# Optimization experiments

Measured on AMD Instinct MI355X. Metric: run time of the kernel, lower is better.

Reference implementation:

```python
import jax, jax.numpy as jnp
import numpy as np

S, B, H2, V = 2048, 16, 2048, 1024  # seq, batch, 2*hidden_dim, v_dim
ALPHA_S = 0.5


def setup_inputs() -> dict:
    key = jax.random.key(0)
    ks = jax.random.split(key, 8)
    sc_in = 1.0 / np.sqrt(H2)
    sc_v = 1.0 / np.sqrt(V)
    return {
        "hidden": jax.random.normal(ks[0], (S, B, H2), dtype=jnp.float32),
        "z": jax.random.normal(ks[1], (S, B, H2), dtype=jnp.float32),
        "Ww": jax.random.normal(ks[2], (H2, V), dtype=jnp.float32) * sc_in,
        "bw": jax.random.normal(ks[3], (V,), dtype=jnp.float32) * sc_in,
        "Wz": jax.random.normal(ks[4], (H2, V), dtype=jnp.float32) * sc_in,
        "bz": jax.random.normal(ks[5], (V,), dtype=jnp.float32) * sc_in,
        "Vw": jax.random.normal(ks[6], (V, 1), dtype=jnp.float32) * sc_v,
        "vb": jax.random.normal(ks[7], (1,), dtype=jnp.float32) * sc_v,
        "w_a": jnp.zeros((), dtype=jnp.float32),
    }


def reference(hidden, z, Ww, bw, Wz, bz, Vw, vb, w_a):
    # sum_w = w_w(hidden) + w_z(z) + w_a * alpha_s   -> [S, B, V]
    sum_w = (jnp.einsum("sbh,hv->sbv", hidden, Ww) + bw
             + jnp.einsum("sbh,hv->sbv", z, Wz) + bz
             + w_a * ALPHA_S)
    # u = v(tanh(sum_w))                              -> [S, B, 1]
    u = jnp.einsum("sbv,vo->sbo", jnp.tanh(sum_w), Vw) + vb
    # softmax over the sequence (dim 0)
    attention = jax.nn.softmax(u, axis=0)
    return attention
```

## Files before the change

kernel.cpp:

```cpp
#include <hip/hip_runtime.h>
#include <hip/hip_bf16.h>
#include <stdint.h>

#define S_DIM 2048
#define B_DIM 16
#define H2_DIM 2048
#define V_DIM 1024
#define M_DIM (S_DIM * B_DIM)
#define K_HALF 2048
#define K_TOT 4096

typedef __attribute__((ext_vector_type(8))) short s16x8;
typedef __attribute__((ext_vector_type(4))) float f32x4;

__device__ __forceinline__ uint16_t f2bf(float f) {
    union { float f; uint32_t u; } c; c.f = f;
    uint32_t u = c.u;
    u += 0x7fffu + ((u >> 16) & 1u);
    return (uint16_t)(u >> 16);
}

__device__ __forceinline__ uint32_t pack_bf16_rn(float a, float b) {
    union { float f; uint32_t u; } ca, cb; ca.f = a; cb.f = b;
    uint32_t ua = ca.u + 0x8000u;
    uint32_t ub = cb.u + 0x8000u;
    return __builtin_amdgcn_perm(ub, ua, 0x07060302u);
}

__device__ __forceinline__ float fast_tanh(float x) {
    float e = __expf(2.0f * x);
    return 1.0f - 2.0f / (e + 1.0f);
}

__device__ __forceinline__ void gload_lds16(const void* g, void* l) {
    __builtin_amdgcn_global_load_lds(
        (__attribute__((address_space(1))) void*)(uintptr_t)g,
        (__attribute__((address_space(3))) void*)(uint32_t)(uintptr_t)l,
        16, 0, 0);
}

__global__ void transposeB(const float* __restrict__ Ww, const float* __restrict__ Wz,
                           uint16_t* __restrict__ B1, uint16_t* __restrict__ B2) {
    __shared__ float tile[32][33];
    const float* src = blockIdx.z ? Wz : Ww;
    uint16_t* dst = blockIdx.z ? B2 : B1;
    int k0 = blockIdx.x * 32, v0 = blockIdx.y * 32;
    int tv = threadIdx.x & 31, tk = threadIdx.x >> 5;
#pragma unroll
    for (int r = 0; r < 4; r++) {
        int k = tk * 4 + r;
        tile[k][tv] = src[(size_t)(k0 + k) * V_DIM + v0 + tv];
    }
    __syncthreads();
#pragma unroll
    for (int r = 0; r < 4; r++) {
        int v = tk * 4 + r;
        dst[(size_t)(v0 + v) * K_HALF + k0 + tv] = f2bf(tile[tv][v]);
    }
}

__global__ __launch_bounds__(256, 2) void gemm_kernel(
    const float* __restrict__ F1, const float* __restrict__ F2,
    const uint16_t* __restrict__ B1, const uint16_t* __restrict__ B2,
    const float* __restrict__ bw, const float* __restrict__ bz,
    const float* __restrict__ wa_p, const float* __restrict__ Vw,
    float* __restrict__ u) {
    __shared__ __align__(16) uint16_t lA[128 * 64];
    __shared__ __align__(16) uint16_t lB[256 * 64];

    const int tid = threadIdx.x;
    const int lane = tid & 63;
    const int wv = tid >> 6;
    const int wm = (wv >> 1) * 64, wn = (wv & 1) * 128;
    const int id = blockIdx.x;
    const int nBase = ((id >> 3) & 3) * 256;
    const int mBase = ((id & 7) + ((id >> 5) << 3)) * 128;
    const int lr = lane >> 3;
    const int lc = lane & 7;
    const int cg = lc ^ lr;
    const int col = lane & 15, quad = lane >> 4;

    f32x4 acc[4][8] = {};

    for (int kb = 0; kb < K_TOT; kb += 64) {
        const int kcol = kb & (K_HALF - 1);
        const float* Fb = (kb < K_HALF) ? F1 : F2;
        const uint16_t* Bb = (kb < K_HALF) ? B1 : B2;

        __syncthreads();

#pragma unroll
        for (int j = 0; j < 8; j++) {
            const int rb = wv * 64 + j * 8;
            const uint16_t* gb = Bb + (size_t)(nBase + rb + lr) * K_HALF + kcol + cg * 8;
            gload_lds16(gb, &lB[rb * 64]);
        }
#pragma unroll
        for (int j = 0; j < 4; j++) {
            const int rb = wv * 32 + j * 8;
            const float* gp = Fb + (size_t)(mBase + rb + lr) * K_HALF + kcol + cg * 8;
            float4 x = ((const float4*)gp)[0];
            float4 y = ((const float4*)gp)[1];
            uint32_t p0 = pack_bf16_rn(x.x, x.y);
            uint32_t p1 = pack_bf16_rn(x.z, x.w);
            uint32_t p2 = pack_bf16_rn(y.x, y.y);
            uint32_t p3 = pack_bf16_rn(y.z, y.w);
            *(uint4*)&lA[rb * 64 + lane * 8] = make_uint4(p0, p1, p2, p3);
        }
        __syncthreads();

#pragma unroll
        for (int kk = 0; kk < 2; kk++) {
            s16x8 af[4], bf[8];
            const int cidx = kk * 4 + quad;
#pragma unroll
            for (int i = 0; i < 4; i++) {
                int m = wm + i * 16 + col;
                af[i] = *(const s16x8*)&lA[m * 64 + ((cidx ^ (m & 7)) << 3)];
            }
#pragma unroll
            for (int j = 0; j < 8; j++) {
                int n = wn + j * 16 + col;
                bf[j] = *(const s16x8*)&lB[n * 64 + ((cidx ^ (n & 7)) << 3)];
            }
#pragma unroll
            for (int i = 0; i < 4; i++)
#pragma unroll
                for (int j = 0; j < 8; j++)
                    acc[i][j] = __builtin_amdgcn_mfma_f32_16x16x32_bf16(af[i], bf[j], acc[i][j], 0, 0, 0);
        }
    }

    const float wa05 = wa_p[0] * 0.5f;
    float biasv[8], vwv[8];
#pragma unroll
    for (int j = 0; j < 8; j++) {
        int n = nBase + wn + j * 16 + col;
        biasv[j] = bw[n] + bz[n] + wa05;
        vwv[j] = Vw[n];
    }
#pragma unroll
    for (int i = 0; i < 4; i++) {
#pragma unroll
        for (int r = 0; r < 4; r++) {
            float s = 0.f;
#pragma unroll
            for (int j = 0; j < 8; j++) {
                float xv = acc[i][j][r] + biasv[j];
                s += fast_tanh(xv) * vwv[j];
            }
            s += __shfl_xor(s, 8);
            s += __shfl_xor(s, 4);
            s += __shfl_xor(s, 2);
            s += __shfl_xor(s, 1);
            if (col == 0)
                atomicAdd(&u[mBase + wm + i * 16 + quad * 4 + r], s);
        }
    }
}

__global__ void softmax_kernel(float* __restrict__ u) {
    const int b = blockIdx.x;
    const int t = threadIdx.x;
    __shared__ float redm[4], reds[4];
    float v[8];
    float mx = -1e30f;
#pragma unroll
    for (int k = 0; k < 8; k++) {
        v[k] = u[(size_t)(t + k * 256) * B_DIM + b];
        mx = fmaxf(mx, v[k]);
    }
#pragma unroll
    for (int off = 32; off >= 1; off >>= 1) mx = fmaxf(mx, __shfl_xor(mx, off));
    if ((t & 63) == 0) redm[t >> 6] = mx;
    __syncthreads();
    mx = fmaxf(fmaxf(redm[0], redm[1]), fmaxf(redm[2], redm[3]));
    float s = 0.f;
#pragma unroll
    for (int k = 0; k < 8; k++) {
        v[k] = __expf(v[k] - mx);
        s += v[k];
    }
#pragma unroll
    for (int off = 32; off >= 1; off >>= 1) s += __shfl_xor(s, off);
    if ((t & 63) == 0) reds[t >> 6] = s;
    __syncthreads();
    s = reds[0] + reds[1] + reds[2] + reds[3];
    float inv = 1.0f / s;
#pragma unroll
    for (int k = 0; k < 8; k++)
        u[(size_t)(t + k * 256) * B_DIM + b] = v[k] * inv;
}

extern "C" void kernel_launch(void* const* d_in, const int* in_sizes, int n_in,
                              void* d_out, int out_size, void* d_ws, size_t ws_size,
                              hipStream_t stream) {
    const float* hidden = (const float*)d_in[0];
    const float* z = (const float*)d_in[1];
    const float* Ww = (const float*)d_in[2];
    const float* bw = (const float*)d_in[3];
    const float* Wz = (const float*)d_in[4];
    const float* bz = (const float*)d_in[5];
    const float* Vw = (const float*)d_in[6];
    const float* wa = (const float*)d_in[8];
    float* out = (float*)d_out;

    char* ws = (char*)d_ws;
    const size_t bBytes = (size_t)V_DIM * K_HALF * 2;
    uint16_t* wsB1 = (uint16_t*)ws;
    uint16_t* wsB2 = (uint16_t*)(ws + bBytes);

    hipMemsetAsync(d_out, 0, (size_t)M_DIM * sizeof(float), stream);

    transposeB<<<dim3(K_HALF / 32, V_DIM / 32, 2), 256, 0, stream>>>(Ww, Wz, wsB1, wsB2);

    gemm_kernel<<<dim3((M_DIM / 128) * (V_DIM / 256)), 256, 0, stream>>>(
        hidden, z, wsB1, wsB2, bw, bz, wa, Vw, out);

    softmax_kernel<<<B_DIM, 256, 0, stream>>>(out);
}
```

Measured before the change: 770.2 us.

## Load A fragments directly to registers and double-buffer B tile in LDS

The GEMM tile shrinks from 128x256 to 128x128, and each wave now owns 32 rows and the full 128 columns. A fragments are loaded from global fp32 straight into registers and converted to bf16 there, which removes the A staging in LDS. B is double-buffered in LDS, with the next tile prefetched via global_load_lds while the current one is consumed, and one barrier per iteration instead of two. Occupancy target rises to 3 blocks per CU. The trade-off is that each A element is now read by twice as many blocks (8 N-tiles instead of 4), and the A loads are less coalesced.

```diff
diff --git a/kernel.cpp b/kernel.cpp
--- a/kernel.cpp
+++ b/kernel.cpp
@@ -27,6 +27,13 @@
     return __builtin_amdgcn_perm(ub, ua, 0x07060302u);
 }
 
+__device__ __forceinline__ s16x8 pack8(float4 x, float4 y) {
+    union { uint4 u; s16x8 v; } r;
+    r.u = make_uint4(pack_bf16_rn(x.x, x.y), pack_bf16_rn(x.z, x.w),
+                     pack_bf16_rn(y.x, y.y), pack_bf16_rn(y.z, y.w));
+    return r.v;
+}
+
 __device__ __forceinline__ float fast_tanh(float x) {
     float e = __expf(2.0f * x);
     return 1.0f - 2.0f / (e + 1.0f);
@@ -59,75 +66,89 @@
     }
 }
 
-__global__ __launch_bounds__(256, 2) void gemm_kernel(
+__global__ __launch_bounds__(256, 3) void gemm_kernel(
     const float* __restrict__ F1, const float* __restrict__ F2,
     const uint16_t* __restrict__ B1, const uint16_t* __restrict__ B2,
     const float* __restrict__ bw, const float* __restrict__ bz,
     const float* __restrict__ wa_p, const float* __restrict__ Vw,
     float* __restrict__ u) {
-    __shared__ __align__(16) uint16_t lA[128 * 64];
-    __shared__ __align__(16) uint16_t lB[256 * 64];
+    __shared__ __align__(16) uint16_t lB[2][128 * 64];
 
     const int tid = threadIdx.x;
     const int lane = tid & 63;
     const int wv = tid >> 6;
-    const int wm = (wv >> 1) * 64, wn = (wv & 1) * 128;
     const int id = blockIdx.x;
-    const int nBase = ((id >> 3) & 3) * 256;
-    const int mBase = ((id & 7) + ((id >> 5) << 3)) * 128;
+    const int nBase = ((id >> 3) & 7) * 128;
+    const int mBase = ((id & 7) + ((id >> 6) << 3)) * 128;
+    const int col = lane & 15, quad = lane >> 4;
     const int lr = lane >> 3;
     const int lc = lane & 7;
     const int cg = lc ^ lr;
-    const int col = lane & 15, quad = lane >> 4;
-
-    f32x4 acc[4][8] = {};
-
-    for (int kb = 0; kb < K_TOT; kb += 64) {
+
+    f32x4 acc[2][8] = {};
+
+    const size_t rowOff = (size_t)(mBase + wv * 32 + col) * K_HALF + quad * 8;
+    const float* a0h[2] = { F1 + rowOff, F2 + rowOff };
+    const float* a1h[2] = { F1 + rowOff + (size_t)16 * K_HALF, F2 + rowOff + (size_t)16 * K_HALF };
+
+#pragma unroll
+    for (int j = 0; j < 4; j++) {
+        const int rb = wv * 32 + j * 8;
+        gload_lds16(B1 + (size_t)(nBase + rb + lr) * K_HALF + cg * 8, &lB[0][rb * 64]);
+    }
+
+#pragma unroll 2
+    for (int s = 0; s < 64; s++) {
+        const int kb = s * 64;
         const int kcol = kb & (K_HALF - 1);
-        const float* Fb = (kb < K_HALF) ? F1 : F2;
-        const uint16_t* Bb = (kb < K_HALF) ? B1 : B2;
+        const int half = (kb < K_HALF) ? 0 : 1;
 
         __syncthreads();
 
-#pragma unroll
-        for (int j = 0; j < 8; j++) {
-            const int rb = wv * 64 + j * 8;
-            const uint16_t* gb = Bb + (size_t)(nBase + rb + lr) * K_HALF + kcol + cg * 8;
-            gload_lds16(gb, &lB[rb * 64]);
+        const float* a0 = a0h[half] + kcol;
+        const float* a1 = a1h[half] + kcol;
+        float4 x00 = ((const float4*)a0)[0];
+        float4 y00 = ((const float4*)a0)[1];
+        float4 x10 = ((const float4*)a1)[0];
+        float4 y10 = ((const float4*)a1)[1];
+        float4 x01 = ((const float4*)(a0 + 32))[0];
+        float4 y01 = ((const float4*)(a0 + 32))[1];
+        float4 x11 = ((const float4*)(a1 + 32))[0];
+        float4 y11 = ((const float4*)(a1 + 32))[1];
+
+        if (s + 1 < 64) {
+            const int kb2 = kb + 64;
+            const int kcol2 = kb2 & (K_HALF - 1);
+            const uint16_t* Bb = (kb2 < K_HALF) ? B1 : B2;
+            uint16_t* dst = lB[(s + 1) & 1];
+#pragma unroll
+            for (int j = 0; j < 4; j++) {
+                const int rb = wv * 32 + j * 8;
+                gload_lds16(Bb + (size_t)(nBase + rb + lr) * K_HALF + kcol2 + cg * 8, &dst[rb * 64]);
+            }
         }
-#pragma unroll
-        for (int j = 0; j < 4; j++) {
-            const int rb = wv * 32 + j * 8;
-            const float* gp = Fb + (size_t)(mBase + rb + lr) * K_HALF + kcol + cg * 8;
-            float4 x = ((const float4*)gp)[0];
-            float4 y = ((const float4*)gp)[1];
-            uint32_t p0 = pack_bf16_rn(x.x, x.y);
-            uint32_t p1 = pack_bf16_rn(x.z, x.w);
-            uint32_t p2 = pack_bf16_rn(y.x, y.y);
-            uint32_t p3 = pack_bf16_rn(y.z, y.w);
-            *(uint4*)&lA[rb * 64 + lane * 8] = make_uint4(p0, p1, p2, p3);
-        }
-        __syncthreads();
+
+        const uint16_t* lb = lB[s & 1];
+        s16x8 af[2][2];
+        af[0][0] = pack8(x00, y00);
+        af[1][0] = pack8(x10, y10);
+        af[0][1] = pack8(x01, y01);
+        af[1][1] = pack8(x11, y11);
 
 #pragma unroll
         for (int kk = 0; kk < 2; kk++) {
-            s16x8 af[4], bf[8];
+            s16x8 bf[8];
             const int cidx = kk * 4 + quad;
 #pragma unroll
-            for (int i = 0; i < 4; i++) {
-                int m = wm + i * 16 + col;
-                af[i] = *(const s16x8*)&lA[m * 64 + ((cidx ^ (m & 7)) << 3)];
-            }
-#pragma unroll
             for (int j = 0; j < 8; j++) {
-                int n = wn + j * 16 + col;
-                bf[j] = *(const s16x8*)&lB[n * 64 + ((cidx ^ (n & 7)) << 3)];
-            }
-#pragma unroll
-            for (int i = 0; i < 4; i++)
-#pragma unroll
-                for (int j = 0; j < 8; j++)
-                    acc[i][j] = __builtin_amdgcn_mfma_f32_16x16x32_bf16(af[i], bf[j], acc[i][j], 0, 0, 0);
+                int n = j * 16 + col;
+                bf[j] = *(const s16x8*)&lb[n * 64 + ((cidx ^ (n & 7)) << 3)];
+            }
+#pragma unroll
+            for (int j = 0; j < 8; j++) {
+                acc[0][j] = __builtin_amdgcn_mfma_f32_16x16x32_bf16(af[0][kk], bf[j], acc[0][j], 0, 0, 0);
+                acc[1][j] = __builtin_amdgcn_mfma_f32_16x16x32_bf16(af[1][kk], bf[j], acc[1][j], 0, 0, 0);
+            }
         }
     }
 
@@ -135,26 +156,26 @@
     float biasv[8], vwv[8];
 #pragma unroll
     for (int j = 0; j < 8; j++) {
-        int n = nBase + wn + j * 16 + col;
+        int n = nBase + j * 16 + col;
         biasv[j] = bw[n] + bz[n] + wa05;
         vwv[j] = Vw[n];
     }
 #pragma unroll
-    for (int i = 0; i < 4; i++) {
+    for (int i = 0; i < 2; i++) {
 #pragma unroll
         for (int r = 0; r < 4; r++) {
-            float s = 0.f;
+            float sv = 0.f;
 #pragma unroll
             for (int j = 0; j < 8; j++) {
                 float xv = acc[i][j][r] + biasv[j];
-                s += fast_tanh(xv) * vwv[j];
-            }
-            s += __shfl_xor(s, 8);
-            s += __shfl_xor(s, 4);
-            s += __shfl_xor(s, 2);
-            s += __shfl_xor(s, 1);
+                sv += fast_tanh(xv) * vwv[j];
+            }
+            sv += __shfl_xor(sv, 8);
+            sv += __shfl_xor(sv, 4);
+            sv += __shfl_xor(sv, 2);
+            sv += __shfl_xor(sv, 1);
             if (col == 0)
-                atomicAdd(&u[mBase + wm + i * 16 + quad * 4 + r], s);
+                atomicAdd(&u[mBase + wv * 32 + i * 16 + quad * 4 + r], sv);
         }
     }
 }
@@ -214,7 +235,7 @@
 
     transposeB<<<dim3(K_HALF / 32, V_DIM / 32, 2), 256, 0, stream>>>(Ww, Wz, wsB1, wsB2);
 
-    gemm_kernel<<<dim3((M_DIM / 128) * (V_DIM / 256)), 256, 0, stream>>>(
+    gemm_kernel<<<dim3((M_DIM / 128) * (V_DIM / 128)), 256, 0, stream>>>(
         hidden, z, wsB1, wsB2, bw, bz, wa, Vw, out);
 
     softmax_kernel<<<B_DIM, 256, 0, stream>>>(out);
```

After: 994.3 us. 1.29x slower.

## Double-buffer B tiles and prefetch A registers one k-step ahead in GEMM

Applied to the files above, without the earlier changes.

Restructures the GEMM main loop into a software pipeline. Next-step A loads (fp32 into registers) and B global-to-LDS loads are issued before the current MFMA work, with B held in two LDS buffers and a manual vmcnt wait. This is meant to hide global memory latency behind compute. It raises LDS use and register pressure and depends on hand-written waitcnt and barrier sequencing.

```diff
diff --git a/kernel.cpp b/kernel.cpp
--- a/kernel.cpp
+++ b/kernel.cpp
@@ -66,7 +66,7 @@
     const float* __restrict__ wa_p, const float* __restrict__ Vw,
     float* __restrict__ u) {
     __shared__ __align__(16) uint16_t lA[128 * 64];
-    __shared__ __align__(16) uint16_t lB[256 * 64];
+    __shared__ __align__(16) uint16_t lB[2][256 * 64];
 
     const int tid = threadIdx.x;
     const int lane = tid & 63;
@@ -82,33 +82,59 @@
 
     f32x4 acc[4][8] = {};
 
-    for (int kb = 0; kb < K_TOT; kb += 64) {
-        const int kcol = kb & (K_HALF - 1);
-        const float* Fb = (kb < K_HALF) ? F1 : F2;
-        const uint16_t* Bb = (kb < K_HALF) ? B1 : B2;
-
-        __syncthreads();
-
-#pragma unroll
-        for (int j = 0; j < 8; j++) {
-            const int rb = wv * 64 + j * 8;
-            const uint16_t* gb = Bb + (size_t)(nBase + rb + lr) * K_HALF + kcol + cg * 8;
-            gload_lds16(gb, &lB[rb * 64]);
-        }
+    const float* aRow[2];
+    const uint16_t* bRow[2];
+    {
+        const size_t aoff = (size_t)(mBase + wv * 32 + lr) * K_HALF + cg * 8;
+        aRow[0] = F1 + aoff; aRow[1] = F2 + aoff;
+        const size_t boff = (size_t)(nBase + wv * 64 + lr) * K_HALF + cg * 8;
+        bRow[0] = B1 + boff; bRow[1] = B2 + boff;
+    }
+
+    float4 ar[4][2];
+
+    auto loadA = [&](int kb) {
+        const float* base = aRow[kb >> 11] + (kb & (K_HALF - 1));
 #pragma unroll
         for (int j = 0; j < 4; j++) {
-            const int rb = wv * 32 + j * 8;
-            const float* gp = Fb + (size_t)(mBase + rb + lr) * K_HALF + kcol + cg * 8;
-            float4 x = ((const float4*)gp)[0];
-            float4 y = ((const float4*)gp)[1];
-            uint32_t p0 = pack_bf16_rn(x.x, x.y);
-            uint32_t p1 = pack_bf16_rn(x.z, x.w);
-            uint32_t p2 = pack_bf16_rn(y.x, y.y);
-            uint32_t p3 = pack_bf16_rn(y.z, y.w);
-            *(uint4*)&lA[rb * 64 + lane * 8] = make_uint4(p0, p1, p2, p3);
-        }
-        __syncthreads();
-
+            const float* gp = base + (size_t)(j * 8) * K_HALF;
+            ar[j][0] = ((const float4*)gp)[0];
+            ar[j][1] = ((const float4*)gp)[1];
+        }
+    };
+    auto issueB = [&](int kb, int p) {
+        const uint16_t* base = bRow[kb >> 11] + (kb & (K_HALF - 1));
+#pragma unroll
+        for (int j = 0; j < 8; j++)
+            gload_lds16(base + (size_t)(j * 8) * K_HALF, &lB[p][(wv * 64 + j * 8) * 64]);
+    };
+
+    loadA(0);
+    issueB(0, 0);
+
+#pragma unroll 1
+    for (int s = 0; s < 64; s++) {
+        const int p = s & 1;
+
+#pragma unroll
+        for (int j = 0; j < 4; j++) {
+            uint4 w = make_uint4(pack_bf16_rn(ar[j][0].x, ar[j][0].y),
+                                 pack_bf16_rn(ar[j][0].z, ar[j][0].w),
+                                 pack_bf16_rn(ar[j][1].x, ar[j][1].y),
+                                 pack_bf16_rn(ar[j][1].z, ar[j][1].w));
+            *(uint4*)&lA[(wv * 32 + j * 8 + lr) * 64 + lc * 8] = w;
+        }
+
+        if (s < 63) {
+            const int kb2 = (s + 1) * 64;
+            loadA(kb2);
+            issueB(kb2, p ^ 1);
+            asm volatile("s_waitcnt vmcnt(16) lgkmcnt(0)\n\ts_barrier" ::: "memory");
+        } else {
+            asm volatile("s_waitcnt vmcnt(0) lgkmcnt(0)\n\ts_barrier" ::: "memory");
+        }
+
+        const uint16_t* lb = lB[p];
 #pragma unroll
         for (int kk = 0; kk < 2; kk++) {
             s16x8 af[4], bf[8];
@@ -121,7 +147,7 @@
 #pragma unroll
             for (int j = 0; j < 8; j++) {
                 int n = wn + j * 16 + col;
-                bf[j] = *(const s16x8*)&lB[n * 64 + ((cidx ^ (n & 7)) << 3)];
+                bf[j] = *(const s16x8*)&lb[n * 64 + ((cidx ^ (n & 7)) << 3)];
             }
 #pragma unroll
             for (int i = 0; i < 4; i++)
@@ -129,6 +155,7 @@
                 for (int j = 0; j < 8; j++)
                     acc[i][j] = __builtin_amdgcn_mfma_f32_16x16x32_bf16(af[i], bf[j], acc[i][j], 0, 0, 0);
         }
+        asm volatile("s_barrier" ::: "memory");
     }
 
     const float wa05 = wa_p[0] * 0.5f;
@@ -143,18 +170,18 @@
     for (int i = 0; i < 4; i++) {
 #pragma unroll
         for (int r = 0; r < 4; r++) {
-            float s = 0.f;
+            float sv = 0.f;
 #pragma unroll
             for (int j = 0; j < 8; j++) {
                 float xv = acc[i][j][r] + biasv[j];
-                s += fast_tanh(xv) * vwv[j];
+                sv += fast_tanh(xv) * vwv[j];
             }
-            s += __shfl_xor(s, 8);
-            s += __shfl_xor(s, 4);
-            s += __shfl_xor(s, 2);
-            s += __shfl_xor(s, 1);
+            sv += __shfl_xor(sv, 8);
+            sv += __shfl_xor(sv, 4);
+            sv += __shfl_xor(sv, 2);
+            sv += __shfl_xor(sv, 1);
             if (col == 0)
-                atomicAdd(&u[mBase + wm + i * 16 + quad * 4 + r], s);
+                atomicAdd(&u[mBase + wm + i * 16 + quad * 4 + r], sv);
         }
     }
 }
```

Measured after the change: 711.8 us. 1.08x faster.
